# Performance work log

Hardware: AMD Instinct MI355X
Metric: run time of the kernel (lower is better)

## Reference

```python
import jax, jax.numpy as jnp
import numpy as np

DIM = 384
B, H, W = 32, 32, 32


def setup_inputs() -> dict:
    key = jax.random.key(0)
    ks = jax.random.split(key, 10)
    s = 1.0 / np.sqrt(DIM)  # conv-like init scale
    return {
        "rgb_feat": jax.random.normal(ks[0], (B, DIM, H, W), dtype=jnp.float32),
        "ms_feat": jax.random.normal(ks[1], (B, DIM, H, W), dtype=jnp.float32),
        "Wq": jax.random.normal(ks[2], (DIM, DIM), dtype=jnp.float32) * s,
        "bq": jax.random.normal(ks[3], (DIM,), dtype=jnp.float32) * s,
        "Wk": jax.random.normal(ks[4], (DIM, DIM), dtype=jnp.float32) * s,
        "bk": jax.random.normal(ks[5], (DIM,), dtype=jnp.float32) * s,
        "Wv": jax.random.normal(ks[6], (DIM, DIM), dtype=jnp.float32) * s,
        "bv": jax.random.normal(ks[7], (DIM,), dtype=jnp.float32) * s,
        "Wf": jax.random.normal(ks[8], (DIM, DIM), dtype=jnp.float32) * s,
        "bf": jax.random.normal(ks[9], (DIM,), dtype=jnp.float32) * s,
    }


def _proj(x_bcn, Wdc, b_d):
    # 1x1 conv == channel-mixing linear: (b,c,n) -> (b,d,n)
    return jnp.einsum('dc,bcn->bdn', Wdc, x_bcn) + b_d[None, :, None]


def reference(rgb_feat, ms_feat, Wq, bq, Wk, bk, Wv, bv, Wf, bf):
    b, c, h, w = rgb_feat.shape
    n = h * w
    rgb = rgb_feat.reshape(b, c, n)
    ms = ms_feat.reshape(b, c, n)

    q = _proj(rgb, Wq, bq)   # (b, c, n)
    k = _proj(ms, Wk, bk)    # (b, c, n)
    v = _proj(ms, Wv, bv)    # (b, c, n)

    scale = 1.0 / jnp.sqrt(jnp.asarray(c, dtype=q.dtype))
    # scores: (b, n_q, n_k) == bmm(q^T, k) / sqrt(c)
    scores = jnp.einsum('bcn,bcm->bnm', q, k) * scale
    attn = jax.nn.softmax(scores, axis=-1)
    # out: (b, n, c) == bmm(attn, v^T); back to (b, c, n)
    out = jnp.einsum('bnm,bcm->bcn', attn, v)

    fused = _proj(out, Wf, bf)  # final 1x1 conv
    return fused.reshape(b, c, h, w)
```

## Files before the change

kernel.cpp:

```cpp
#include <hip/hip_runtime.h>

#define DIMC 384
#define NTOK 1024
#define BATCH 32
#define KT12 12

using short8 = __attribute__((ext_vector_type(8))) short;
using f32x4  = __attribute__((ext_vector_type(4))) float;
using uint4_ = __attribute__((ext_vector_type(4))) unsigned int;
typedef unsigned short u16;

#define MFMA16 __builtin_amdgcn_mfma_f32_16x16x32_bf16

#define GLD_LDS16(gp, lp)                                                     \
    __builtin_amdgcn_global_load_lds(                                         \
        (const __attribute__((address_space(1))) void*)(gp),                  \
        (__attribute__((address_space(3))) void*)(lp), 16, 0, 0)

__device__ __forceinline__ u16 f2bf(float f) {
    unsigned int u = __builtin_bit_cast(unsigned int, f);
    u += 0x7FFFu + ((u >> 16) & 1u);
    return (u16)(u >> 16);
}
__device__ __forceinline__ float bf2f(u16 h) {
    unsigned int u = ((unsigned int)h) << 16;
    return __builtin_bit_cast(float, u);
}


__global__ __launch_bounds__(256) void transpose_sw(
    const float* __restrict__ X, u16* __restrict__ Xsw)
{
    __shared__ float tl[64 * 65];
    const int b = blockIdx.z, n0 = blockIdx.x * 64, c0 = blockIdx.y * 64;
    const int t = threadIdx.x;

#pragma unroll
    for (int p = 0; p < 4; ++p) {
        int idx = p * 256 + t;
        int c = idx >> 4, n4 = (idx & 15) * 4;
        f32x4 v = *(const f32x4*)(X + ((size_t)b * DIMC + c0 + c) * NTOK + n0 + n4);
#pragma unroll
        for (int i = 0; i < 4; ++i) tl[c * 65 + n4 + i] = v[i];
    }
    __syncthreads();
    u16* dstb = Xsw + (size_t)b * NTOK * DIMC;
#pragma unroll
    for (int p = 0; p < 2; ++p) {
        int g = p * 256 + t;
        int n15 = g & 15, quad = (g >> 4) & 3, ktl = (g >> 6) & 1, rg = g >> 7;
        int c8 = ktl * 32 + quad * 8;
        int nl = rg * 16 + n15;
        uint4_ pk;
#pragma unroll
        for (int i = 0; i < 4; ++i) {
            u16 lo = f2bf(tl[(c8 + 2 * i) * 65 + nl]);
            u16 hi = f2bf(tl[(c8 + 2 * i + 1) * 65 + nl]);
            pk[i] = (unsigned)lo | ((unsigned)hi << 16);
        }
        size_t dst = (((size_t)(n0 >> 4) + rg) * KT12 + (c0 >> 5) + ktl) * 512 + (size_t)(g & 63) * 8;
        *(uint4_*)(dstb + dst) = pk;
    }
}

__global__ __launch_bounds__(256) void wcvt_sw(
    const float* __restrict__ w0, const float* __restrict__ w1,
    const float* __restrict__ w2, const float* __restrict__ w3,
    u16* __restrict__ dst, float s0)
{
    const float* srcs[4] = {w0, w1, w2, w3};
    const float* s = srcs[blockIdx.y];
    float scl = (blockIdx.y == 0) ? s0 : 1.0f;
    u16* d = dst + (size_t)blockIdx.y * DIMC * DIMC;
    int e0 = (blockIdx.x * 256 + threadIdx.x) * 8;
    int dd = e0 / DIMC, c8 = e0 % DIMC;
    f32x4 a = *(const f32x4*)(s + e0);
    f32x4 b2 = *(const f32x4*)(s + e0 + 4);
    uint4_ pk;
    pk[0] = (unsigned)f2bf(a[0] * scl) | ((unsigned)f2bf(a[1] * scl) << 16);
    pk[1] = (unsigned)f2bf(a[2] * scl) | ((unsigned)f2bf(a[3] * scl) << 16);
    pk[2] = (unsigned)f2bf(b2[0] * scl) | ((unsigned)f2bf(b2[1] * scl) << 16);
    pk[3] = (unsigned)f2bf(b2[2] * scl) | ((unsigned)f2bf(b2[3] * scl) << 16);
    size_t off = ((size_t)(dd >> 4) * KT12 + (c8 >> 5)) * 512 +
                 (size_t)((((c8 >> 3) & 3) * 16 + (dd & 15)) * 8);
    *(uint4_*)(d + off) = pk;
}

__global__ __launch_bounds__(256) void proj3_sw(
    const u16* __restrict__ rgb_sw, const u16* __restrict__ ms_sw,
    const u16* __restrict__ w_sw,
    u16* __restrict__ q_sw, u16* __restrict__ k_sw, u16* __restrict__ v_sw,
    const float* __restrict__ bq, const float* __restrict__ bk,
    const float* __restrict__ bv, float s0)
{
    __shared__ __align__(16) u16 t16[128 * 76];
    const int s = blockIdx.y, b = blockIdx.z, tile = blockIdx.x;
    const size_t TB = (size_t)NTOK * DIMC, WN = (size_t)DIMC * DIMC;
    const u16 *A, *B; u16* O; const float* bias;
    int ktd, bRow, r0, c0; float bsc = 1.f;
    if (s == 0) {
        A = rgb_sw + b * TB; B = w_sw; O = q_sw + b * TB; bias = bq;
        ktd = 12; bRow = 0; r0 = (tile / 6) * 128; c0 = (tile % 6) * 64; bsc = s0;
    } else if (s == 1) {
        A = ms_sw + b * TB; B = w_sw + WN; O = k_sw + b * TB; bias = bk;
        ktd = 12; bRow = 0; r0 = (tile / 6) * 128; c0 = (tile % 6) * 64;
    } else {
        A = w_sw + 2 * WN; B = ms_sw + b * TB; O = v_sw + b * TB; bias = bv;
        ktd = 32; bRow = 1; r0 = (tile / 16) * 128; c0 = (tile % 16) * 64;
    }

    const int t = threadIdx.x, w = t >> 6, lane = t & 63;
    const int l15 = lane & 15, quad = lane >> 4;

    f32x4 acc[2][4];
#pragma unroll
    for (int ss = 0; ss < 2; ++ss)
#pragma unroll
        for (int mc = 0; mc < 4; ++mc) acc[ss][mc] = (f32x4){0.f, 0.f, 0.f, 0.f};

    const u16* aP = A + ((size_t)(r0 >> 4) + w * 2) * (KT12 * 512) + (size_t)lane * 8;
    const u16* bP = B + (size_t)(c0 >> 4) * (KT12 * 512) + (size_t)lane * 8;
#pragma unroll
    for (int dk = 0; dk < 12; ++dk) {
        short8 a0 = *(const short8*)(aP + dk * 512);
        short8 a1 = *(const short8*)(aP + (KT12 + dk) * 512);
#pragma unroll
        for (int mc = 0; mc < 4; ++mc) {
            short8 bf = *(const short8*)(bP + ((size_t)mc * KT12 + dk) * 512);
            acc[0][mc] = MFMA16(a0, bf, acc[0][mc], 0, 0, 0);
            acc[1][mc] = MFMA16(a1, bf, acc[1][mc], 0, 0, 0);
        }
    }

    if (bRow) {
#pragma unroll
        for (int ss = 0; ss < 2; ++ss) {
            f32x4 bv4 = *(const f32x4*)(bias + r0 + w * 32 + ss * 16 + quad * 4);
#pragma unroll
            for (int mc = 0; mc < 4; ++mc)
#pragma unroll
                for (int r = 0; r < 4; ++r) acc[ss][mc][r] += bv4[r];
        }
    } else {
#pragma unroll
        for (int mc = 0; mc < 4; ++mc) {
            float bc = bias[c0 + mc * 16 + l15] * bsc;
#pragma unroll
            for (int ss = 0; ss < 2; ++ss)
#pragma unroll
                for (int r = 0; r < 4; ++r) acc[ss][mc][r] += bc;
        }
    }

#pragma unroll
    for (int ss = 0; ss < 2; ++ss)
#pragma unroll
        for (int mc = 0; mc < 4; ++mc)
#pragma unroll
            for (int r = 0; r < 4; ++r)
                t16[(w * 32 + ss * 16 + quad * 4 + r) * 76 + mc * 16 + l15] = f2bf(acc[ss][mc][r]);
    __syncthreads();
#pragma unroll
    for (int p = 0; p < 4; ++p) {
        int g = p * 256 + t;
        int lan = g & 63, ktl = (g >> 6) & 1, rg = g >> 7;
        int row = rg * 16 + (lan & 15);
        int col = ktl * 32 + ((lan >> 4) & 3) * 8;
        uint4_ v = *(const uint4_*)(t16 + row * 76 + col);
        size_t dst = (((size_t)(r0 >> 4) + rg) * ktd + (c0 >> 5) + ktl) * 512 + (size_t)lan * 8;
        *(uint4_*)(O + dst) = v;
    }
}

__global__ __launch_bounds__(256) void projf_sw(
    const u16* __restrict__ wf_sw, const u16* __restrict__ osw,
    const float* __restrict__ bfp, float* __restrict__ out)
{
    __shared__ __align__(16) float t32[128 * 68];
    const int b = blockIdx.y, tile = blockIdx.x;
    const int r0 = (tile / 16) * 128, c0 = (tile % 16) * 64;
    const size_t TB = (size_t)NTOK * DIMC;

    const int t = threadIdx.x, w = t >> 6, lane = t & 63;
    const int quad = lane >> 4;

    f32x4 acc[2][4];
#pragma unroll
    for (int ss = 0; ss < 2; ++ss)
#pragma unroll
        for (int mc = 0; mc < 4; ++mc) acc[ss][mc] = (f32x4){0.f, 0.f, 0.f, 0.f};

    const u16* aP = wf_sw + ((size_t)(r0 >> 4) + w * 2) * (KT12 * 512) + (size_t)lane * 8;
    const u16* bP = osw + (size_t)b * TB + (size_t)(c0 >> 4) * (KT12 * 512) + (size_t)lane * 8;
#pragma unroll
    for (int dk = 0; dk < 12; ++dk) {
        short8 a0 = *(const short8*)(aP + dk * 512);
        short8 a1 = *(const short8*)(aP + (KT12 + dk) * 512);
#pragma unroll
        for (int mc = 0; mc < 4; ++mc) {
            short8 bf = *(const short8*)(bP + ((size_t)mc * KT12 + dk) * 512);
            acc[0][mc] = MFMA16(a0, bf, acc[0][mc], 0, 0, 0);
            acc[1][mc] = MFMA16(a1, bf, acc[1][mc], 0, 0, 0);
        }
    }
#pragma unroll
    for (int ss = 0; ss < 2; ++ss) {
        f32x4 bv4 = *(const f32x4*)(bfp + r0 + w * 32 + ss * 16 + quad * 4);
#pragma unroll
        for (int mc = 0; mc < 4; ++mc)
#pragma unroll
            for (int r = 0; r < 4; ++r) acc[ss][mc][r] += bv4[r];
    }

#pragma unroll
    for (int ss = 0; ss < 2; ++ss)
#pragma unroll
        for (int mc = 0; mc < 4; ++mc)
#pragma unroll
            for (int r = 0; r < 4; ++r)
                t32[(w * 32 + ss * 16 + quad * 4 + r) * 68 + mc * 16 + (lane & 15)] = acc[ss][mc][r];
    __syncthreads();
    float* Ob = out + (size_t)b * DIMC * NTOK;
#pragma unroll
    for (int p = 0; p < 8; ++p) {
        int g = p * 256 + t;
        int row = g >> 4, c4 = (g & 15) * 4;
        f32x4 v = *(const f32x4*)(t32 + row * 68 + c4);
        *(f32x4*)(Ob + (size_t)(r0 + row) * NTOK + c0 + c4) = v;
    }
}

__global__ __launch_bounds__(512, 2) void attn_lds(
    const u16* __restrict__ qsw, const u16* __restrict__ ksw,
    const u16* __restrict__ vsw, u16* __restrict__ osw)
{
    __shared__ __align__(16) u16 smem[58880];

    const int bid = blockIdx.x;
    const int b = (bid & 7) * 4 + ((bid >> 3) & 3);
    const int qb = bid >> 5;
    const int t = threadIdx.x, w = t >> 6, lane = t & 63;
    const int l15 = lane & 15, quad = lane >> 4;
    const int rt = qb * 8 + w;

    const size_t TB = (size_t)NTOK * DIMC;
    const u16* kb = ksw + (size_t)b * TB;
    const u16* vb = vsw + (size_t)b * TB;
    u16* pw = smem + 49152 + w * 1216;

    short8 qf[12];
    const u16* qp = qsw + (size_t)b * TB + (size_t)rt * (KT12 * 512) + (size_t)lane * 8;
#pragma unroll
    for (int dk = 0; dk < 12; ++dk) qf[dk] = *(const short8*)(qp + dk * 512);

    f32x4 Oa[24];
#pragma unroll
    for (int i = 0; i < 24; ++i) Oa[i] = (f32x4){0.f, 0.f, 0.f, 0.f};
    float m_run[4], l_run[4];
#pragma unroll
    for (int r = 0; r < 4; ++r) { m_run[r] = -1e30f; l_run[r] = 0.f; }

    const int i0 = w * 3;

#pragma unroll
    for (int j = 0; j < 3; ++j) {
        int idx = i0 + j;
        GLD_LDS16(kb + (size_t)idx * 512 + lane * 8, smem + idx * 512);
        GLD_LDS16(vb + (size_t)(idx * 32) * 512 + lane * 8, smem + 24576 + idx * 512);
    }
    __syncthreads();

    for (int mt = 0; mt < 32; ++mt) {
        const int cur = mt & 1;
        u16* kcur = smem + cur * 12288;
        u16* vcur = smem + 24576 + cur * 12288;

        if (mt < 31) {
            u16* knxt = smem + (cur ^ 1) * 12288;
            u16* vnxt = smem + 24576 + (cur ^ 1) * 12288;
#pragma unroll
            for (int j = 0; j < 3; ++j) {
                int idx = i0 + j;
                GLD_LDS16(kb + (size_t)(24 * (mt + 1) + idx) * 512 + lane * 8,
                          knxt + idx * 512);
                GLD_LDS16(vb + (size_t)(idx * 32 + mt + 1) * 512 + lane * 8,
                          vnxt + idx * 512);
            }
        }

        f32x4 s[2];
        s[0] = (f32x4){0.f, 0.f, 0.f, 0.f};
        s[1] = (f32x4){0.f, 0.f, 0.f, 0.f};
        const u16* kfb = kcur + (size_t)lane * 8;
        __builtin_amdgcn_s_setprio(1);
#pragma unroll
        for (int dk = 0; dk < 12; ++dk) {
            short8 k0 = *(const short8*)(kfb + dk * 512);
            short8 k1 = *(const short8*)(kfb + (12 + dk) * 512);
            s[0] = MFMA16(qf[dk], k0, s[0], 0, 0, 0);
            s[1] = MFMA16(qf[dk], k1, s[1], 0, 0, 0);
        }
        __builtin_amdgcn_s_setprio(0);

        float mx4[4];
#pragma unroll
        for (int r = 0; r < 4; ++r) {
            float mx = fmaxf(s[0][r], s[1][r]);
            mx = fmaxf(mx, __shfl_xor(mx, 1));
            mx = fmaxf(mx, __shfl_xor(mx, 2));
            mx = fmaxf(mx, __shfl_xor(mx, 4));
            mx = fmaxf(mx, __shfl_xor(mx, 8));
            mx4[r] = mx;
        }
        int grow = (mx4[0] > m_run[0] + 8.f) | (mx4[1] > m_run[1] + 8.f) |
                   (mx4[2] > m_run[2] + 8.f) | (mx4[3] > m_run[3] + 8.f);
        if (__any(grow)) {
            float alpha[4];
#pragma unroll
            for (int r = 0; r < 4; ++r) {
                float mn = fmaxf(m_run[r], mx4[r]);
                alpha[r] = exp2f(m_run[r] - mn);
                m_run[r] = mn;
                l_run[r] *= alpha[r];
            }
#pragma unroll
            for (int ci = 0; ci < 24; ++ci)
#pragma unroll
                for (int r = 0; r < 4; ++r) Oa[ci][r] *= alpha[r];
        }
#pragma unroll
        for (int r = 0; r < 4; ++r) {
            float ls = 0.f;
#pragma unroll
            for (int mc = 0; mc < 2; ++mc) {
                float p = exp2f(s[mc][r] - m_run[r]);
                u16 pb = f2bf(p);
                pw[(quad * 4 + r) * 76 + mc * 16 + l15] = pb;
                ls += bf2f(pb);
            }
            ls += __shfl_xor(ls, 1);
            ls += __shfl_xor(ls, 2);
            ls += __shfl_xor(ls, 4);
            ls += __shfl_xor(ls, 8);
            l_run[r] += ls;
        }

        short8 pa = *(const short8*)(pw + l15 * 76 + quad * 8);
        const u16* vfb = vcur + (size_t)lane * 8;
        __builtin_amdgcn_s_setprio(1);
#pragma unroll
        for (int ci = 0; ci < 24; ++ci) {
            short8 vf = *(const short8*)(vfb + ci * 512);
            Oa[ci] = MFMA16(pa, vf, Oa[ci], 0, 0, 0);
        }
        __builtin_amdgcn_s_setprio(0);

        __syncthreads();
    }

    float rl[4];
#pragma unroll
    for (int r = 0; r < 4; ++r) rl[r] = 1.f / l_run[r];
    u16* od = osw + (size_t)b * TB;
#pragma unroll
    for (int ch = 0; ch < 6; ++ch) {
#pragma unroll
        for (int cc = 0; cc < 4; ++cc)
#pragma unroll
            for (int r = 0; r < 4; ++r)
                pw[(quad * 4 + r) * 76 + cc * 16 + l15] = f2bf(Oa[ch * 4 + cc][r] * rl[r]);
#pragma unroll
        for (int ktl = 0; ktl < 2; ++ktl) {
            uint4_ vv = *(const uint4_*)(pw + l15 * 76 + ktl * 32 + quad * 8);
            size_t dst = ((size_t)rt * KT12 + ch * 2 + ktl) * 512 + (size_t)lane * 8;
            *(uint4_*)(od + dst) = vv;
        }
    }
}

extern "C" void kernel_launch(void* const* d_in, const int* in_sizes, int n_in,
                              void* d_out, int out_size, void* d_ws, size_t ws_size,
                              hipStream_t stream) {
    const float* rgb = (const float*)d_in[0];
    const float* ms  = (const float*)d_in[1];
    const float* Wq  = (const float*)d_in[2];
    const float* bq  = (const float*)d_in[3];
    const float* Wk  = (const float*)d_in[4];
    const float* bk  = (const float*)d_in[5];
    const float* Wv  = (const float*)d_in[6];
    const float* bv  = (const float*)d_in[7];
    const float* Wf  = (const float*)d_in[8];
    const float* bf_ = (const float*)d_in[9];
    float* outp = (float*)d_out;

    const float SC2 = 0.05103103630798288f * 1.4426950408889634f;

    const size_t TN = (size_t)BATCH * NTOK * DIMC;
    const size_t WN = (size_t)DIMC * DIMC;
    u16* rgb_sw = (u16*)d_ws;
    u16* ms_sw  = rgb_sw + TN;
    u16* q_sw   = ms_sw + TN;
    u16* k_sw   = q_sw + TN;
    u16* v_sw   = k_sw + TN;
    u16* o_sw   = v_sw + TN;
    u16* w_sw   = o_sw + TN;

    wcvt_sw<<<dim3(72, 4), 256, 0, stream>>>(Wq, Wk, Wv, Wf, w_sw, SC2);
    transpose_sw<<<dim3(16, 6, BATCH), 256, 0, stream>>>(rgb, rgb_sw);
    transpose_sw<<<dim3(16, 6, BATCH), 256, 0, stream>>>(ms, ms_sw);

    proj3_sw<<<dim3(48, 3, BATCH), 256, 0, stream>>>(
        rgb_sw, ms_sw, w_sw, q_sw, k_sw, v_sw, bq, bk, bv, SC2);

    attn_lds<<<dim3(256), 512, 0, stream>>>(q_sw, k_sw, v_sw, o_sw);

    projf_sw<<<dim3(48, BATCH), 256, 0, stream>>>(w_sw + 3 * WN, o_sw, bf_, outp);
}
```

Before: 344.5 us.

## Retile projection GEMMs to 128x128 with double-buffered LDS staging

The Q/K/V and final projection kernels move from 128x64 tiles that each wave loaded straight from global memory to 128x128 tiles. A and B k-slices are now staged into LDS through double-buffered global_load_lds, and each wave computes a 64x64 sub-tile with a 4x4 MFMA accumulator grid. The grid is flattened with batch in the low bits and the epilogue writes per wave (projf writes fp32 directly, without an LDS transpose). The aim is better operand reuse and overlap of loads with MFMA, at the cost of more accumulator registers and a barrier per k-step, and the projf output writes are less coalesced.

```diff
diff --git a/kernel.cpp b/kernel.cpp
--- a/kernel.cpp
+++ b/kernel.cpp
@@ -86,147 +86,196 @@
     *(uint4_*)(d + off) = pk;
 }
 
-__global__ __launch_bounds__(256) void proj3_sw(
+__global__ __launch_bounds__(256, 3) void proj3_g(
     const u16* __restrict__ rgb_sw, const u16* __restrict__ ms_sw,
     const u16* __restrict__ w_sw,
     u16* __restrict__ q_sw, u16* __restrict__ k_sw, u16* __restrict__ v_sw,
     const float* __restrict__ bq, const float* __restrict__ bk,
     const float* __restrict__ bv, float s0)
 {
-    __shared__ __align__(16) u16 t16[128 * 76];
-    const int s = blockIdx.y, b = blockIdx.z, tile = blockIdx.x;
+    __shared__ __align__(16) u16 smem[21248];
+
+    const int bid = blockIdx.x;
+    const int b = bid & 31;
+    const int rr = bid >> 5;
+    const int s = rr % 3, tile = rr / 3;
     const size_t TB = (size_t)NTOK * DIMC, WN = (size_t)DIMC * DIMC;
     const u16 *A, *B; u16* O; const float* bias;
     int ktd, bRow, r0, c0; float bsc = 1.f;
     if (s == 0) {
         A = rgb_sw + b * TB; B = w_sw; O = q_sw + b * TB; bias = bq;
-        ktd = 12; bRow = 0; r0 = (tile / 6) * 128; c0 = (tile % 6) * 64; bsc = s0;
+        ktd = 12; bRow = 0; r0 = (tile & 7) * 128; c0 = (tile >> 3) * 128; bsc = s0;
     } else if (s == 1) {
         A = ms_sw + b * TB; B = w_sw + WN; O = k_sw + b * TB; bias = bk;
-        ktd = 12; bRow = 0; r0 = (tile / 6) * 128; c0 = (tile % 6) * 64;
+        ktd = 12; bRow = 0; r0 = (tile & 7) * 128; c0 = (tile >> 3) * 128;
     } else {
         A = w_sw + 2 * WN; B = ms_sw + b * TB; O = v_sw + b * TB; bias = bv;
-        ktd = 32; bRow = 1; r0 = (tile / 16) * 128; c0 = (tile % 16) * 64;
+        ktd = 32; bRow = 1; r0 = (tile % 3) * 128; c0 = (tile / 3) * 128;
     }
 
     const int t = threadIdx.x, w = t >> 6, lane = t & 63;
     const int l15 = lane & 15, quad = lane >> 4;
-
-    f32x4 acc[2][4];
-#pragma unroll
-    for (int ss = 0; ss < 2; ++ss)
-#pragma unroll
-        for (int mc = 0; mc < 4; ++mc) acc[ss][mc] = (f32x4){0.f, 0.f, 0.f, 0.f};
-
-    const u16* aP = A + ((size_t)(r0 >> 4) + w * 2) * (KT12 * 512) + (size_t)lane * 8;
-    const u16* bP = B + (size_t)(c0 >> 4) * (KT12 * 512) + (size_t)lane * 8;
-#pragma unroll
-    for (int dk = 0; dk < 12; ++dk) {
-        short8 a0 = *(const short8*)(aP + dk * 512);
-        short8 a1 = *(const short8*)(aP + (KT12 + dk) * 512);
-#pragma unroll
-        for (int mc = 0; mc < 4; ++mc) {
-            short8 bf = *(const short8*)(bP + ((size_t)mc * KT12 + dk) * 512);
-            acc[0][mc] = MFMA16(a0, bf, acc[0][mc], 0, 0, 0);
-            acc[1][mc] = MFMA16(a1, bf, acc[1][mc], 0, 0, 0);
-        }
+    const int wr = w >> 1, wc = w & 1;
+    const int rt0 = r0 >> 4, ct0 = c0 >> 4;
+    u16* pw = smem + 16384 + w * 1216;
+
+    f32x4 acc[4][4];
+#pragma unroll
+    for (int ai = 0; ai < 4; ++ai)
+#pragma unroll
+        for (int bj = 0; bj < 4; ++bj) acc[ai][bj] = (f32x4){0.f, 0.f, 0.f, 0.f};
+
+    {
+        const u16* As = A + ((size_t)(rt0 + 2 * w) * KT12) * 512 + (size_t)lane * 8;
+        GLD_LDS16(As, smem + (2 * w) * 512);
+        GLD_LDS16(As + KT12 * 512, smem + (2 * w + 1) * 512);
+        const u16* Bs = B + ((size_t)(ct0 + 2 * w) * KT12) * 512 + (size_t)lane * 8;
+        GLD_LDS16(Bs, smem + 8192 + (2 * w) * 512);
+        GLD_LDS16(Bs + KT12 * 512, smem + 8192 + (2 * w + 1) * 512);
+    }
+    __syncthreads();
+
+    for (int kt = 0; kt < 12; ++kt) {
+        const int cur = kt & 1;
+        if (kt < 11) {
+            u16* dA = smem + (cur ^ 1) * 4096;
+            u16* dB = smem + 8192 + (cur ^ 1) * 4096;
+            const u16* As = A + ((size_t)(rt0 + 2 * w) * KT12 + kt + 1) * 512 + (size_t)lane * 8;
+            GLD_LDS16(As, dA + (2 * w) * 512);
+            GLD_LDS16(As + KT12 * 512, dA + (2 * w + 1) * 512);
+            const u16* Bs = B + ((size_t)(ct0 + 2 * w) * KT12 + kt + 1) * 512 + (size_t)lane * 8;
+            GLD_LDS16(Bs, dB + (2 * w) * 512);
+            GLD_LDS16(Bs + KT12 * 512, dB + (2 * w + 1) * 512);
+        }
+        const u16* sA = smem + cur * 4096 + (size_t)(wr * 4) * 512 + (size_t)lane * 8;
+        const u16* sB = smem + 8192 + cur * 4096 + (size_t)(wc * 4) * 512 + (size_t)lane * 8;
+        short8 aF[4], bF[4];
+#pragma unroll
+        for (int ai = 0; ai < 4; ++ai) aF[ai] = *(const short8*)(sA + ai * 512);
+#pragma unroll
+        for (int bj = 0; bj < 4; ++bj) bF[bj] = *(const short8*)(sB + bj * 512);
+        __builtin_amdgcn_s_setprio(1);
+#pragma unroll
+        for (int ai = 0; ai < 4; ++ai)
+#pragma unroll
+            for (int bj = 0; bj < 4; ++bj)
+                acc[ai][bj] = MFMA16(aF[ai], bF[bj], acc[ai][bj], 0, 0, 0);
+        __builtin_amdgcn_s_setprio(0);
+        __syncthreads();
     }
 
     if (bRow) {
 #pragma unroll
-        for (int ss = 0; ss < 2; ++ss) {
-            f32x4 bv4 = *(const f32x4*)(bias + r0 + w * 32 + ss * 16 + quad * 4);
-#pragma unroll
-            for (int mc = 0; mc < 4; ++mc)
-#pragma unroll
-                for (int r = 0; r < 4; ++r) acc[ss][mc][r] += bv4[r];
+        for (int ai = 0; ai < 4; ++ai) {
+            f32x4 bv4 = *(const f32x4*)(bias + r0 + wr * 64 + ai * 16 + quad * 4);
+#pragma unroll
+            for (int bj = 0; bj < 4; ++bj)
+#pragma unroll
+                for (int r = 0; r < 4; ++r) acc[ai][bj][r] += bv4[r];
         }
     } else {
 #pragma unroll
-        for (int mc = 0; mc < 4; ++mc) {
-            float bc = bias[c0 + mc * 16 + l15] * bsc;
-#pragma unroll
-            for (int ss = 0; ss < 2; ++ss)
-#pragma unroll
-                for (int r = 0; r < 4; ++r) acc[ss][mc][r] += bc;
-        }
-    }
-
-#pragma unroll
-    for (int ss = 0; ss < 2; ++ss)
-#pragma unroll
-        for (int mc = 0; mc < 4; ++mc)
+        for (int bj = 0; bj < 4; ++bj) {
+            float bc = bias[c0 + wc * 64 + bj * 16 + l15] * bsc;
+#pragma unroll
+            for (int ai = 0; ai < 4; ++ai)
+#pragma unroll
+                for (int r = 0; r < 4; ++r) acc[ai][bj][r] += bc;
+        }
+    }
+
+#pragma unroll
+    for (int ai = 0; ai < 4; ++ai) {
+#pragma unroll
+        for (int bj = 0; bj < 4; ++bj)
 #pragma unroll
             for (int r = 0; r < 4; ++r)
-                t16[(w * 32 + ss * 16 + quad * 4 + r) * 76 + mc * 16 + l15] = f2bf(acc[ss][mc][r]);
-    __syncthreads();
-#pragma unroll
-    for (int p = 0; p < 4; ++p) {
-        int g = p * 256 + t;
-        int lan = g & 63, ktl = (g >> 6) & 1, rg = g >> 7;
-        int row = rg * 16 + (lan & 15);
-        int col = ktl * 32 + ((lan >> 4) & 3) * 8;
-        uint4_ v = *(const uint4_*)(t16 + row * 76 + col);
-        size_t dst = (((size_t)(r0 >> 4) + rg) * ktd + (c0 >> 5) + ktl) * 512 + (size_t)lan * 8;
-        *(uint4_*)(O + dst) = v;
-    }
-}
-
-__global__ __launch_bounds__(256) void projf_sw(
+                pw[(quad * 4 + r) * 76 + bj * 16 + l15] = f2bf(acc[ai][bj][r]);
+        const int rt = rt0 + wr * 4 + ai;
+        const int kb0 = (c0 + wc * 64) >> 5;
+#pragma unroll
+        for (int ktl = 0; ktl < 2; ++ktl) {
+            uint4_ v = *(const uint4_*)(pw + l15 * 76 + ktl * 32 + quad * 8);
+            *(uint4_*)(O + ((size_t)rt * ktd + kb0 + ktl) * 512 + (size_t)lane * 8) = v;
+        }
+    }
+}
+
+__global__ __launch_bounds__(256, 3) void projf_g(
     const u16* __restrict__ wf_sw, const u16* __restrict__ osw,
     const float* __restrict__ bfp, float* __restrict__ out)
 {
-    __shared__ __align__(16) float t32[128 * 68];
-    const int b = blockIdx.y, tile = blockIdx.x;
-    const int r0 = (tile / 16) * 128, c0 = (tile % 16) * 64;
+    __shared__ __align__(16) u16 smem[16384];
+    const int bid = blockIdx.x;
+    const int b = bid & 31, tile = bid >> 5;
+    const int r0 = (tile % 3) * 128, c0 = (tile / 3) * 128;
     const size_t TB = (size_t)NTOK * DIMC;
 
     const int t = threadIdx.x, w = t >> 6, lane = t & 63;
-    const int quad = lane >> 4;
-
-    f32x4 acc[2][4];
-#pragma unroll
-    for (int ss = 0; ss < 2; ++ss)
-#pragma unroll
-        for (int mc = 0; mc < 4; ++mc) acc[ss][mc] = (f32x4){0.f, 0.f, 0.f, 0.f};
-
-    const u16* aP = wf_sw + ((size_t)(r0 >> 4) + w * 2) * (KT12 * 512) + (size_t)lane * 8;
-    const u16* bP = osw + (size_t)b * TB + (size_t)(c0 >> 4) * (KT12 * 512) + (size_t)lane * 8;
-#pragma unroll
-    for (int dk = 0; dk < 12; ++dk) {
-        short8 a0 = *(const short8*)(aP + dk * 512);
-        short8 a1 = *(const short8*)(aP + (KT12 + dk) * 512);
-#pragma unroll
-        for (int mc = 0; mc < 4; ++mc) {
-            short8 bf = *(const short8*)(bP + ((size_t)mc * KT12 + dk) * 512);
-            acc[0][mc] = MFMA16(a0, bf, acc[0][mc], 0, 0, 0);
-            acc[1][mc] = MFMA16(a1, bf, acc[1][mc], 0, 0, 0);
-        }
-    }
-#pragma unroll
-    for (int ss = 0; ss < 2; ++ss) {
-        f32x4 bv4 = *(const f32x4*)(bfp + r0 + w * 32 + ss * 16 + quad * 4);
-#pragma unroll
-        for (int mc = 0; mc < 4; ++mc)
-#pragma unroll
-            for (int r = 0; r < 4; ++r) acc[ss][mc][r] += bv4[r];
-    }
-
-#pragma unroll
-    for (int ss = 0; ss < 2; ++ss)
-#pragma unroll
-        for (int mc = 0; mc < 4; ++mc)
-#pragma unroll
-            for (int r = 0; r < 4; ++r)
-                t32[(w * 32 + ss * 16 + quad * 4 + r) * 68 + mc * 16 + (lane & 15)] = acc[ss][mc][r];
+    const int l15 = lane & 15, quad = lane >> 4;
+    const int wr = w >> 1, wc = w & 1;
+    const int rt0 = r0 >> 4, ct0 = c0 >> 4;
+    const u16* A = wf_sw;
+    const u16* B = osw + (size_t)b * TB;
+
+    f32x4 acc[4][4];
+#pragma unroll
+    for (int ai = 0; ai < 4; ++ai)
+#pragma unroll
+        for (int bj = 0; bj < 4; ++bj) acc[ai][bj] = (f32x4){0.f, 0.f, 0.f, 0.f};
+
+    {
+        const u16* As = A + ((size_t)(rt0 + 2 * w) * KT12) * 512 + (size_t)lane * 8;
+        GLD_LDS16(As, smem + (2 * w) * 512);
+        GLD_LDS16(As + KT12 * 512, smem + (2 * w + 1) * 512);
+        const u16* Bs = B + ((size_t)(ct0 + 2 * w) * KT12) * 512 + (size_t)lane * 8;
+        GLD_LDS16(Bs, smem + 8192 + (2 * w) * 512);
+        GLD_LDS16(Bs + KT12 * 512, smem + 8192 + (2 * w + 1) * 512);
+    }
     __syncthreads();
+
+    for (int kt = 0; kt < 12; ++kt) {
+        const int cur = kt & 1;
+        if (kt < 11) {
+            u16* dA = smem + (cur ^ 1) * 4096;
+            u16* dB = smem + 8192 + (cur ^ 1) * 4096;
+            const u16* As = A + ((size_t)(rt0 + 2 * w) * KT12 + kt + 1) * 512 + (size_t)lane * 8;
+            GLD_LDS16(As, dA + (2 * w) * 512);
+            GLD_LDS16(As + KT12 * 512, dA + (2 * w + 1) * 512);
+            const u16* Bs = B + ((size_t)(ct0 + 2 * w) * KT12 + kt + 1) * 512 + (size_t)lane * 8;
+            GLD_LDS16(Bs, dB + (2 * w) * 512);
+            GLD_LDS16(Bs + KT12 * 512, dB + (2 * w + 1) * 512);
+        }
+        const u16* sA = smem + cur * 4096 + (size_t)(wr * 4) * 512 + (size_t)lane * 8;
+        const u16* sB = smem + 8192 + cur * 4096 + (size_t)(wc * 4) * 512 + (size_t)lane * 8;
+        short8 aF[4], bF[4];
+#pragma unroll
+        for (int ai = 0; ai < 4; ++ai) aF[ai] = *(const short8*)(sA + ai * 512);
+#pragma unroll
+        for (int bj = 0; bj < 4; ++bj) bF[bj] = *(const short8*)(sB + bj * 512);
+        __builtin_amdgcn_s_setprio(1);
+#pragma unroll
+        for (int ai = 0; ai < 4; ++ai)
+#pragma unroll
+            for (int bj = 0; bj < 4; ++bj)
+                acc[ai][bj] = MFMA16(aF[ai], bF[bj], acc[ai][bj], 0, 0, 0);
+        __builtin_amdgcn_s_setprio(0);
+        __syncthreads();
+    }
+
     float* Ob = out + (size_t)b * DIMC * NTOK;
 #pragma unroll
-    for (int p = 0; p < 8; ++p) {
-        int g = p * 256 + t;
-        int row = g >> 4, c4 = (g & 15) * 4;
-        f32x4 v = *(const f32x4*)(t32 + row * 68 + c4);
-        *(f32x4*)(Ob + (size_t)(r0 + row) * NTOK + c0 + c4) = v;
+    for (int ai = 0; ai < 4; ++ai) {
+        f32x4 bv4 = *(const f32x4*)(bfp + r0 + wr * 64 + ai * 16 + quad * 4);
+#pragma unroll
+        for (int bj = 0; bj < 4; ++bj) {
+            const int col = c0 + wc * 64 + bj * 16 + l15;
+#pragma unroll
+            for (int r = 0; r < 4; ++r) {
+                const int row = r0 + wr * 64 + ai * 16 + quad * 4 + r;
+                Ob[(size_t)row * NTOK + col] = acc[ai][bj][r] + bv4[r];
+            }
+        }
     }
 }
 
@@ -409,10 +458,10 @@
     transpose_sw<<<dim3(16, 6, BATCH), 256, 0, stream>>>(rgb, rgb_sw);
     transpose_sw<<<dim3(16, 6, BATCH), 256, 0, stream>>>(ms, ms_sw);
 
-    proj3_sw<<<dim3(48, 3, BATCH), 256, 0, stream>>>(
+    proj3_g<<<dim3(2304), 256, 0, stream>>>(
         rgb_sw, ms_sw, w_sw, q_sw, k_sw, v_sw, bq, bk, bv, SC2);
 
     attn_lds<<<dim3(256), 512, 0, stream>>>(q_sw, k_sw, v_sw, o_sw);
 
-    projf_sw<<<dim3(48, BATCH), 256, 0, stream>>>(w_sw + 3 * WN, o_sw, bf_, outp);
-}
+    projf_g<<<dim3(768), 256, 0, stream>>>(w_sw + 3 * WN, o_sw, bf_, outp);
+}
```

After: 342.2 us. Within noise of the previous version (-0.7%).
